# Kernel tuning notes

Measured on AMD Instinct MI355X. Metric: run time of the kernel, lower is better.

The kernel has to match this reference:

```python
import jax, jax.numpy as jnp
import numpy as np
import math

L, B, E, H = 1024, 16, 512, 8
NUM_REL = 2 * L - 1  # 2047


def setup_inputs() -> dict:
    key = jax.random.key(0)
    ks = jax.random.split(key, 9)
    s = 0.02
    query = jax.random.normal(ks[0], (L, B, E), dtype=jnp.float32)
    return {
        "query": query,
        "key": jax.random.normal(ks[1], (L, B, E), dtype=jnp.float32),
        "value": jax.random.normal(ks[2], (L, B, E), dtype=jnp.float32),
        "in_proj_weight": jax.random.normal(ks[3], (3 * E, E), dtype=jnp.float32) * s,
        "in_proj_bias": jax.random.normal(ks[4], (3 * E,), dtype=jnp.float32) * s,
        "out_proj_weight": jax.random.normal(ks[5], (E, E), dtype=jnp.float32) * s,
        "out_proj_bias": jax.random.normal(ks[6], (E,), dtype=jnp.float32) * s,
        "rpe_weight_table": jax.random.normal(ks[7], (H, NUM_REL), dtype=jnp.float32) * s,
        "rpe_indices": jax.random.randint(ks[8], (L, L), 0, NUM_REL, dtype=jnp.int32),
    }


def _heads(x, w, b):
    # x: (N, Bn, E), w: (E, E), b: (E,) -> (Bn, H, N, d)
    n, bn, e = x.shape
    d = e // H
    y = jnp.einsum('nbe,fe->nbf', x, w) + b
    return y.reshape(n, bn, H, d).transpose(1, 2, 0, 3)


def reference(query, key, value, in_proj_weight, in_proj_bias, out_proj_weight,
              out_proj_bias, rpe_weight_table, rpe_indices):
    l, bn, e = query.shape
    d = e // H
    wq, wk, wv = jnp.split(in_proj_weight, 3, axis=0)
    bq, bk, bv = jnp.split(in_proj_bias, 3, axis=0)
    q = _heads(query, wq, bq)   # (B, H, L, d)
    k = _heads(key, wk, bk)     # (B, H, S, d)
    v = _heads(value, wv, bv)   # (B, H, S, d)
    q = q / math.sqrt(d)
    # rel-pos bias: gather table -> (H, L, S), broadcast over batch
    bias = rpe_weight_table[:, rpe_indices]
    attn = jnp.einsum('bhld,bhsd->bhls', q, k) + bias[None]
    attn = jax.nn.softmax(attn, axis=-1)
    out = jnp.einsum('bhls,bhsd->bhld', attn, v)   # (B, H, L, d)
    out = out.transpose(2, 0, 1, 3).reshape(l, bn, e)  # (L, B, E)
    out = jnp.einsum('lbe,fe->lbf', out, out_proj_weight) + out_proj_bias
    return out
```

## Files before the change

kernel.cpp:

```cpp
#include <hip/hip_runtime.h>
#include <hip/hip_bf16.h>


#define L_SEQ 1024
#define B_N   16
#define E_DIM 512
#define H_N   8
#define NREL  2047

typedef _Float16 f16;
using half8   = __attribute__((ext_vector_type(8))) _Float16;
using floatx4 = __attribute__((ext_vector_type(4))) float;

__device__ __forceinline__ half8 cvt8(const float4 a, const float4 b) {
    half8 h;
    h[0] = (f16)a.x; h[1] = (f16)a.y; h[2] = (f16)a.z; h[3] = (f16)a.w;
    h[4] = (f16)b.x; h[5] = (f16)b.y; h[6] = (f16)b.z; h[7] = (f16)b.w;
    return h;
}

__global__ __launch_bounds__(256) void qkv_kernel(
    const float* __restrict__ Xq, const float* __restrict__ Xk, const float* __restrict__ Xv,
    const float* __restrict__ W, const float* __restrict__ Bias,
    f16* __restrict__ Qo, f16* __restrict__ Ko, f16* __restrict__ Vo)
{
    const int proj = blockIdx.z;
    const int f0   = blockIdx.x << 7;
    const int n0   = blockIdx.y << 7;
    const float* X  = (proj == 0) ? Xq : (proj == 1) ? Xk : Xv;
    const float* Wp = W + (size_t)(proj << 9) * E_DIM;

    __shared__ __align__(16) f16 As[128][40];
    __shared__ __align__(16) f16 Bs[128][40];

    const int tid  = threadIdx.x;
    const int w    = tid >> 6;
    const int lane = tid & 63;
    const int quad = lane >> 4, c = lane & 15;
    const int wm = (w >> 1) << 6, wn = (w & 1) << 6;

    const int srow = tid >> 1;
    const int sseg = (tid & 1) << 4;

    floatx4 acc[4][4] = {};

    for (int k0 = 0; k0 < E_DIM; k0 += 32) {
        const float* xp = X  + (size_t)(n0 + srow) * E_DIM + k0 + sseg;
        const float* wp = Wp + (size_t)(f0 + srow) * E_DIM + k0 + sseg;
        const float4 x0 = *reinterpret_cast<const float4*>(xp);
        const float4 x1 = *reinterpret_cast<const float4*>(xp + 4);
        const float4 x2 = *reinterpret_cast<const float4*>(xp + 8);
        const float4 x3 = *reinterpret_cast<const float4*>(xp + 12);
        const float4 w0 = *reinterpret_cast<const float4*>(wp);
        const float4 w1 = *reinterpret_cast<const float4*>(wp + 4);
        const float4 w2 = *reinterpret_cast<const float4*>(wp + 8);
        const float4 w3 = *reinterpret_cast<const float4*>(wp + 12);
        __syncthreads();
        *reinterpret_cast<half8*>(&As[srow][sseg])     = cvt8(x0, x1);
        *reinterpret_cast<half8*>(&As[srow][sseg + 8]) = cvt8(x2, x3);
        *reinterpret_cast<half8*>(&Bs[srow][sseg])     = cvt8(w0, w1);
        *reinterpret_cast<half8*>(&Bs[srow][sseg + 8]) = cvt8(w2, w3);
        __syncthreads();

        half8 a[4], bfr[4];
#pragma unroll
        for (int mt = 0; mt < 4; ++mt)
            a[mt] = *reinterpret_cast<const half8*>(&As[wm + mt * 16 + c][quad * 8]);
#pragma unroll
        for (int nt = 0; nt < 4; ++nt)
            bfr[nt] = *reinterpret_cast<const half8*>(&Bs[wn + nt * 16 + c][quad * 8]);
#pragma unroll
        for (int mt = 0; mt < 4; ++mt)
#pragma unroll
            for (int nt = 0; nt < 4; ++nt)
                acc[mt][nt] = __builtin_amdgcn_mfma_f32_16x16x32_f16(a[mt], bfr[nt], acc[mt][nt], 0, 0, 0);
    }

    f16* Dst = (proj == 0) ? Qo : (proj == 1) ? Ko : Vo;
    const float scale = (proj == 0) ? 0.125f : 1.0f;

#pragma unroll
    for (int nt = 0; nt < 4; ++nt) {
        const int fl = f0 + wn + nt * 16 + c;
        const float bj = Bias[(proj << 9) + fl];
        const int h = fl >> 6, d = fl & 63;
#pragma unroll
        for (int mt = 0; mt < 4; ++mt) {
#pragma unroll
            for (int r = 0; r < 4; ++r) {
                const int n = n0 + wm + mt * 16 + quad * 4 + r;
                const int l = n >> 4, b = n & 15;
                Dst[((((size_t)b * H_N + h) * L_SEQ + l) << 6) + d] =
                    (f16)((acc[mt][nt][r] + bj) * scale);
            }
        }
    }
}

__global__ __launch_bounds__(256) void transpose_v(
    const f16* __restrict__ V, f16* __restrict__ Vt)
{
    const int l0 = blockIdx.x << 6;
    const size_t base = (size_t)blockIdx.y << 16;
    __shared__ __align__(16) f16 T[64][72];
    const int tid = threadIdx.x;
    const int r = tid >> 2, co = (tid & 3) << 4;

    const uint4 a0 = *reinterpret_cast<const uint4*>(V + base + (size_t)(l0 + r) * 64 + co);
    const uint4 a1 = *reinterpret_cast<const uint4*>(V + base + (size_t)(l0 + r) * 64 + co + 8);
    *reinterpret_cast<uint4*>(&T[r][co])     = a0;
    *reinterpret_cast<uint4*>(&T[r][co + 8]) = a1;
    __syncthreads();

    union { f16 h[16]; uint4 u[2]; } pk;
#pragma unroll
    for (int j = 0; j < 16; ++j) pk.h[j] = T[co + j][r];
    *reinterpret_cast<uint4*>(Vt + base + (size_t)r * 1024 + l0 + co)     = pk.u[0];
    *reinterpret_cast<uint4*>(Vt + base + (size_t)r * 1024 + l0 + co + 8) = pk.u[1];
}

__global__ __launch_bounds__(256, 3) void attn_kernel(
    const f16* __restrict__ Q, const f16* __restrict__ K, const f16* __restrict__ Vt,
    const int* __restrict__ RPE, const float* __restrict__ Tab, f16* __restrict__ CTX)
{
    const int q0 = blockIdx.x << 7;
    const int bh = blockIdx.y;
    const int b = bh >> 3, h = bh & 7;

    const int tid  = threadIdx.x;
    const int w    = tid >> 6;
    const int lane = tid & 63;
    const int quad = lane >> 4, c = lane & 15;

    __shared__ __align__(16) f16 Ks[64][72];
    __shared__ __align__(16) f16 Vts[64][72];
    __shared__ __align__(16) f16 Pw[4][32][72];
    __shared__ float tab[NREL];

    const size_t base = (size_t)bh << 16;

    for (int i = tid; i < NREL; i += 256) tab[i] = Tab[h * NREL + i];

    const int qg0 = q0 + (w << 5);
    half8 Aq[2][2];
#pragma unroll
    for (int s = 0; s < 2; ++s) {
        const f16* qp = Q + base + (size_t)(qg0 + s * 16 + c) * 64 + quad * 8;
        Aq[s][0] = *reinterpret_cast<const half8*>(qp);
        Aq[s][1] = *reinterpret_cast<const half8*>(qp + 32);
    }

    floatx4 o[2][4] = {};
    float l_part[2][4] = {};

    const int* rp = RPE + (size_t)(qg0 + (quad << 2)) * 1024 + c;

    const int sr = tid >> 2, so = (tid & 3) << 4;
    const f16* kbase = K  + base + (size_t)sr * 64 + so;
    const f16* vbase = Vt + base + (size_t)sr * 1024 + so;

    uint4 pk0 = *reinterpret_cast<const uint4*>(kbase);
    uint4 pk1 = *reinterpret_cast<const uint4*>(kbase + 8);
    uint4 pv0 = *reinterpret_cast<const uint4*>(vbase);
    uint4 pv1 = *reinterpret_cast<const uint4*>(vbase + 8);

    for (int j0 = 0; j0 < L_SEQ; j0 += 64) {
        __syncthreads();
        *reinterpret_cast<uint4*>(&Ks[sr][so])      = pk0;
        *reinterpret_cast<uint4*>(&Ks[sr][so + 8])  = pk1;
        *reinterpret_cast<uint4*>(&Vts[sr][so])     = pv0;
        *reinterpret_cast<uint4*>(&Vts[sr][so + 8]) = pv1;
        __syncthreads();

        if (j0 + 64 < L_SEQ) {
            const f16* kn = kbase + (size_t)(j0 + 64) * 64;
            const f16* vn = vbase + (j0 + 64);
            pk0 = *reinterpret_cast<const uint4*>(kn);
            pk1 = *reinterpret_cast<const uint4*>(kn + 8);
            pv0 = *reinterpret_cast<const uint4*>(vn);
            pv1 = *reinterpret_cast<const uint4*>(vn + 8);
        }

        int idx[2][4][4];
#pragma unroll
        for (int s = 0; s < 2; ++s)
#pragma unroll
            for (int r = 0; r < 4; ++r)
#pragma unroll
                for (int nt = 0; nt < 4; ++nt)
                    idx[s][r][nt] = rp[(size_t)(s * 16 + r) * 1024 + j0 + nt * 16];

        floatx4 sc[2][4];
#pragma unroll
        for (int nt = 0; nt < 4; ++nt) {
            const half8 b0 = *reinterpret_cast<const half8*>(&Ks[nt * 16 + c][quad * 8]);
            const half8 b1 = *reinterpret_cast<const half8*>(&Ks[nt * 16 + c][32 + quad * 8]);
            floatx4 t0 = {}, t1 = {};
            t0 = __builtin_amdgcn_mfma_f32_16x16x32_f16(Aq[0][0], b0, t0, 0, 0, 0);
            t0 = __builtin_amdgcn_mfma_f32_16x16x32_f16(Aq[0][1], b1, t0, 0, 0, 0);
            t1 = __builtin_amdgcn_mfma_f32_16x16x32_f16(Aq[1][0], b0, t1, 0, 0, 0);
            t1 = __builtin_amdgcn_mfma_f32_16x16x32_f16(Aq[1][1], b1, t1, 0, 0, 0);
            sc[0][nt] = t0; sc[1][nt] = t1;
        }

#pragma unroll
        for (int s = 0; s < 2; ++s)
#pragma unroll
            for (int r = 0; r < 4; ++r) {
                float rs = 0.0f;
#pragma unroll
                for (int nt = 0; nt < 4; ++nt) {
                    const float p = __expf(sc[s][nt][r] + tab[idx[s][r][nt]]);
                    rs += p;
                    Pw[w][s * 16 + quad * 4 + r][nt * 16 + c] = (f16)p;
                }
                l_part[s][r] += rs;
            }

        half8 vb[4][2];
#pragma unroll
        for (int nt = 0; nt < 4; ++nt) {
            vb[nt][0] = *reinterpret_cast<const half8*>(&Vts[nt * 16 + c][quad * 8]);
            vb[nt][1] = *reinterpret_cast<const half8*>(&Vts[nt * 16 + c][32 + quad * 8]);
        }
#pragma unroll
        for (int s = 0; s < 2; ++s) {
            const half8 Ap0 = *reinterpret_cast<const half8*>(&Pw[w][s * 16 + c][quad * 8]);
            const half8 Ap1 = *reinterpret_cast<const half8*>(&Pw[w][s * 16 + c][32 + quad * 8]);
#pragma unroll
            for (int nt = 0; nt < 4; ++nt) {
                o[s][nt] = __builtin_amdgcn_mfma_f32_16x16x32_f16(Ap0, vb[nt][0], o[s][nt], 0, 0, 0);
                o[s][nt] = __builtin_amdgcn_mfma_f32_16x16x32_f16(Ap1, vb[nt][1], o[s][nt], 0, 0, 0);
            }
        }
    }

#pragma unroll
    for (int s = 0; s < 2; ++s)
#pragma unroll
        for (int r = 0; r < 4; ++r) {
            float l = l_part[s][r];
            l += __shfl_xor(l, 1); l += __shfl_xor(l, 2);
            l += __shfl_xor(l, 4); l += __shfl_xor(l, 8);
            const float inv = 1.0f / l;
            const int lrow = qg0 + s * 16 + quad * 4 + r;
            f16* dp = CTX + ((size_t)(lrow * 16 + b)) * 512 + h * 64;
#pragma unroll
            for (int nt = 0; nt < 4; ++nt)
                dp[nt * 16 + c] = (f16)(o[s][nt][r] * inv);
        }
}

__global__ __launch_bounds__(256) void out_kernel(
    const f16* __restrict__ X, const float* __restrict__ W, const float* __restrict__ Bias,
    float* __restrict__ Out)
{
    const int f0 = blockIdx.x << 7;
    const int n0 = blockIdx.y << 7;

    __shared__ __align__(16) f16 As[128][40];
    __shared__ __align__(16) f16 Bs[128][40];

    const int tid  = threadIdx.x;
    const int w    = tid >> 6;
    const int lane = tid & 63;
    const int quad = lane >> 4, c = lane & 15;
    const int wm = (w >> 1) << 6, wn = (w & 1) << 6;

    const int srow = tid >> 1;
    const int sseg = (tid & 1) << 4;

    floatx4 acc[4][4] = {};

    for (int k0 = 0; k0 < E_DIM; k0 += 32) {
        const f16* xp = X + (size_t)(n0 + srow) * E_DIM + k0 + sseg;
        const uint4 xu0 = *reinterpret_cast<const uint4*>(xp);
        const uint4 xu1 = *reinterpret_cast<const uint4*>(xp + 8);
        const float* wp = W + (size_t)(f0 + srow) * E_DIM + k0 + sseg;
        const float4 w0 = *reinterpret_cast<const float4*>(wp);
        const float4 w1 = *reinterpret_cast<const float4*>(wp + 4);
        const float4 w2 = *reinterpret_cast<const float4*>(wp + 8);
        const float4 w3 = *reinterpret_cast<const float4*>(wp + 12);
        __syncthreads();
        *reinterpret_cast<uint4*>(&As[srow][sseg])     = xu0;
        *reinterpret_cast<uint4*>(&As[srow][sseg + 8]) = xu1;
        *reinterpret_cast<half8*>(&Bs[srow][sseg])     = cvt8(w0, w1);
        *reinterpret_cast<half8*>(&Bs[srow][sseg + 8]) = cvt8(w2, w3);
        __syncthreads();

        half8 a[4], bfr[4];
#pragma unroll
        for (int mt = 0; mt < 4; ++mt)
            a[mt] = *reinterpret_cast<const half8*>(&As[wm + mt * 16 + c][quad * 8]);
#pragma unroll
        for (int nt = 0; nt < 4; ++nt)
            bfr[nt] = *reinterpret_cast<const half8*>(&Bs[wn + nt * 16 + c][quad * 8]);
#pragma unroll
        for (int mt = 0; mt < 4; ++mt)
#pragma unroll
            for (int nt = 0; nt < 4; ++nt)
                acc[mt][nt] = __builtin_amdgcn_mfma_f32_16x16x32_f16(a[mt], bfr[nt], acc[mt][nt], 0, 0, 0);
    }

#pragma unroll
    for (int nt = 0; nt < 4; ++nt) {
        const int f = f0 + wn + nt * 16 + c;
        const float bj = Bias[f];
#pragma unroll
        for (int mt = 0; mt < 4; ++mt) {
#pragma unroll
            for (int r = 0; r < 4; ++r) {
                const int n = n0 + wm + mt * 16 + quad * 4 + r;
                Out[(size_t)n * E_DIM + f] = acc[mt][nt][r] + bj;
            }
        }
    }
}

extern "C" void kernel_launch(void* const* d_in, const int* in_sizes, int n_in,
                              void* d_out, int out_size, void* d_ws, size_t ws_size,
                              hipStream_t stream) {
    const float* q_in = (const float*)d_in[0];
    const float* k_in = (const float*)d_in[1];
    const float* v_in = (const float*)d_in[2];
    const float* ipw  = (const float*)d_in[3];
    const float* ipb  = (const float*)d_in[4];
    const float* opw  = (const float*)d_in[5];
    const float* opb  = (const float*)d_in[6];
    const float* tab  = (const float*)d_in[7];
    const int*   rpe  = (const int*)d_in[8];
    float* out = (float*)d_out;

    f16* ws   = (f16*)d_ws;
    f16* Q    = ws;
    f16* K    = ws + 8388608;
    f16* Vt   = ws + 16777216;
    f16* Vtmp = ws + 25165824;
    f16* CTX  = ws + 25165824;

    qkv_kernel<<<dim3(4, 128, 3), 256, 0, stream>>>(q_in, k_in, v_in, ipw, ipb, Q, K, Vtmp);
    transpose_v<<<dim3(16, 128), 256, 0, stream>>>(Vtmp, Vt);
    attn_kernel<<<dim3(8, 128), 256, 0, stream>>>(Q, K, Vt, rpe, tab, CTX);
    out_kernel<<<dim3(4, 128), 256, 0, stream>>>(CTX, opw, opb, out);
}
```

Before: 332.3 us.

## Prefetch next K-tile into registers and remap GEMM blocks for XCD locality

The QKV and output projection GEMMs now issue the global loads for the next 32-wide K slice right after the shared-memory stores, so the loads overlap the MFMA work on the current slice instead of stalling at the top of each iteration. Both kernels also switch to a 1D grid whose block index is remapped so that consecutive blocks on the same XCD share the same row tile and its four column tiles. This is meant to improve L2 reuse of the activation rows. It costs extra registers for the prefetch buffers, which may lower occupancy. Only the two projection kernels change; the attention kernel, which likely dominates runtime, is untouched.

```diff
diff --git a/kernel.cpp b/kernel.cpp
--- a/kernel.cpp
+++ b/kernel.cpp
@@ -24,9 +24,14 @@
     const float* __restrict__ W, const float* __restrict__ Bias,
     f16* __restrict__ Qo, f16* __restrict__ Ko, f16* __restrict__ Vo)
 {
-    const int proj = blockIdx.z;
-    const int f0   = blockIdx.x << 7;
-    const int n0   = blockIdx.y << 7;
+    const int flat = blockIdx.x;
+    const int xcd  = flat & 7;
+    const int slot = flat >> 3;
+    const int g    = xcd * 48 + (slot >> 2);
+    const int f0   = (slot & 3) << 7;
+    const int proj = g >> 7;
+    const int n0   = (g & 127) << 7;
+
     const float* X  = (proj == 0) ? Xq : (proj == 1) ? Xk : Xv;
     const float* Wp = W + (size_t)(proj << 9) * E_DIM;
 
@@ -42,25 +47,40 @@
     const int srow = tid >> 1;
     const int sseg = (tid & 1) << 4;
 
+    const float* xrow = X  + (size_t)(n0 + srow) * E_DIM + sseg;
+    const float* wrow = Wp + (size_t)(f0 + srow) * E_DIM + sseg;
+
     floatx4 acc[4][4] = {};
 
+    float4 px0 = *reinterpret_cast<const float4*>(xrow);
+    float4 px1 = *reinterpret_cast<const float4*>(xrow + 4);
+    float4 px2 = *reinterpret_cast<const float4*>(xrow + 8);
+    float4 px3 = *reinterpret_cast<const float4*>(xrow + 12);
+    float4 pw0 = *reinterpret_cast<const float4*>(wrow);
+    float4 pw1 = *reinterpret_cast<const float4*>(wrow + 4);
+    float4 pw2 = *reinterpret_cast<const float4*>(wrow + 8);
+    float4 pw3 = *reinterpret_cast<const float4*>(wrow + 12);
+
     for (int k0 = 0; k0 < E_DIM; k0 += 32) {
-        const float* xp = X  + (size_t)(n0 + srow) * E_DIM + k0 + sseg;
-        const float* wp = Wp + (size_t)(f0 + srow) * E_DIM + k0 + sseg;
-        const float4 x0 = *reinterpret_cast<const float4*>(xp);
-        const float4 x1 = *reinterpret_cast<const float4*>(xp + 4);
-        const float4 x2 = *reinterpret_cast<const float4*>(xp + 8);
-        const float4 x3 = *reinterpret_cast<const float4*>(xp + 12);
-        const float4 w0 = *reinterpret_cast<const float4*>(wp);
-        const float4 w1 = *reinterpret_cast<const float4*>(wp + 4);
-        const float4 w2 = *reinterpret_cast<const float4*>(wp + 8);
-        const float4 w3 = *reinterpret_cast<const float4*>(wp + 12);
-        __syncthreads();
-        *reinterpret_cast<half8*>(&As[srow][sseg])     = cvt8(x0, x1);
-        *reinterpret_cast<half8*>(&As[srow][sseg + 8]) = cvt8(x2, x3);
-        *reinterpret_cast<half8*>(&Bs[srow][sseg])     = cvt8(w0, w1);
-        *reinterpret_cast<half8*>(&Bs[srow][sseg + 8]) = cvt8(w2, w3);
-        __syncthreads();
+        __syncthreads();
+        *reinterpret_cast<half8*>(&As[srow][sseg])     = cvt8(px0, px1);
+        *reinterpret_cast<half8*>(&As[srow][sseg + 8]) = cvt8(px2, px3);
+        *reinterpret_cast<half8*>(&Bs[srow][sseg])     = cvt8(pw0, pw1);
+        *reinterpret_cast<half8*>(&Bs[srow][sseg + 8]) = cvt8(pw2, pw3);
+        __syncthreads();
+
+        if (k0 + 32 < E_DIM) {
+            const float* xn = xrow + k0 + 32;
+            const float* wn2 = wrow + k0 + 32;
+            px0 = *reinterpret_cast<const float4*>(xn);
+            px1 = *reinterpret_cast<const float4*>(xn + 4);
+            px2 = *reinterpret_cast<const float4*>(xn + 8);
+            px3 = *reinterpret_cast<const float4*>(xn + 12);
+            pw0 = *reinterpret_cast<const float4*>(wn2);
+            pw1 = *reinterpret_cast<const float4*>(wn2 + 4);
+            pw2 = *reinterpret_cast<const float4*>(wn2 + 8);
+            pw3 = *reinterpret_cast<const float4*>(wn2 + 12);
+        }
 
         half8 a[4], bfr[4];
 #pragma unroll
@@ -255,8 +275,12 @@
     const f16* __restrict__ X, const float* __restrict__ W, const float* __restrict__ Bias,
     float* __restrict__ Out)
 {
-    const int f0 = blockIdx.x << 7;
-    const int n0 = blockIdx.y << 7;
+    const int flat = blockIdx.x;
+    const int xcd  = flat & 7;
+    const int slot = flat >> 3;
+    const int m    = xcd * 16 + (slot >> 2);
+    const int f0   = (slot & 3) << 7;
+    const int n0   = m << 7;
 
     __shared__ __align__(16) f16 As[128][40];
     __shared__ __align__(16) f16 Bs[128][40];
@@ -270,23 +294,36 @@
     const int srow = tid >> 1;
     const int sseg = (tid & 1) << 4;
 
+    const f16*   xrow = X + (size_t)(n0 + srow) * E_DIM + sseg;
+    const float* wrow = W + (size_t)(f0 + srow) * E_DIM + sseg;
+
     floatx4 acc[4][4] = {};
 
+    uint4  pxu0 = *reinterpret_cast<const uint4*>(xrow);
+    uint4  pxu1 = *reinterpret_cast<const uint4*>(xrow + 8);
+    float4 pw0  = *reinterpret_cast<const float4*>(wrow);
+    float4 pw1  = *reinterpret_cast<const float4*>(wrow + 4);
+    float4 pw2  = *reinterpret_cast<const float4*>(wrow + 8);
+    float4 pw3  = *reinterpret_cast<const float4*>(wrow + 12);
+
     for (int k0 = 0; k0 < E_DIM; k0 += 32) {
-        const f16* xp = X + (size_t)(n0 + srow) * E_DIM + k0 + sseg;
-        const uint4 xu0 = *reinterpret_cast<const uint4*>(xp);
-        const uint4 xu1 = *reinterpret_cast<const uint4*>(xp + 8);
-        const float* wp = W + (size_t)(f0 + srow) * E_DIM + k0 + sseg;
-        const float4 w0 = *reinterpret_cast<const float4*>(wp);
-        const float4 w1 = *reinterpret_cast<const float4*>(wp + 4);
-        const float4 w2 = *reinterpret_cast<const float4*>(wp + 8);
-        const float4 w3 = *reinterpret_cast<const float4*>(wp + 12);
-        __syncthreads();
-        *reinterpret_cast<uint4*>(&As[srow][sseg])     = xu0;
-        *reinterpret_cast<uint4*>(&As[srow][sseg + 8]) = xu1;
-        *reinterpret_cast<half8*>(&Bs[srow][sseg])     = cvt8(w0, w1);
-        *reinterpret_cast<half8*>(&Bs[srow][sseg + 8]) = cvt8(w2, w3);
-        __syncthreads();
+        __syncthreads();
+        *reinterpret_cast<uint4*>(&As[srow][sseg])     = pxu0;
+        *reinterpret_cast<uint4*>(&As[srow][sseg + 8]) = pxu1;
+        *reinterpret_cast<half8*>(&Bs[srow][sseg])     = cvt8(pw0, pw1);
+        *reinterpret_cast<half8*>(&Bs[srow][sseg + 8]) = cvt8(pw2, pw3);
+        __syncthreads();
+
+        if (k0 + 32 < E_DIM) {
+            const f16*   xn = xrow + k0 + 32;
+            const float* wn2 = wrow + k0 + 32;
+            pxu0 = *reinterpret_cast<const uint4*>(xn);
+            pxu1 = *reinterpret_cast<const uint4*>(xn + 8);
+            pw0  = *reinterpret_cast<const float4*>(wn2);
+            pw1  = *reinterpret_cast<const float4*>(wn2 + 4);
+            pw2  = *reinterpret_cast<const float4*>(wn2 + 8);
+            pw3  = *reinterpret_cast<const float4*>(wn2 + 12);
+        }
 
         half8 a[4], bfr[4];
 #pragma unroll
@@ -338,8 +375,8 @@
     f16* Vtmp = ws + 25165824;
     f16* CTX  = ws + 25165824;
 
-    qkv_kernel<<<dim3(4, 128, 3), 256, 0, stream>>>(q_in, k_in, v_in, ipw, ipb, Q, K, Vtmp);
+    qkv_kernel<<<dim3(1536), 256, 0, stream>>>(q_in, k_in, v_in, ipw, ipb, Q, K, Vtmp);
     transpose_v<<<dim3(16, 128), 256, 0, stream>>>(Vtmp, Vt);
     attn_kernel<<<dim3(8, 128), 256, 0, stream>>>(Q, K, Vt, rpe, tab, CTX);
-    out_kernel<<<dim3(4, 128), 256, 0, stream>>>(CTX, opw, opb, out);
-}
+    out_kernel<<<dim3(512), 256, 0, stream>>>(CTX, opw, opb, out);
+}
```

Measured after the change: 321.2 us. 3.3% less time.
